# Kernel optimization log

Hardware: AMD Instinct MI355X
Metric: run time of the kernel (lower is better)

Reference implementation:

```python
import jax, jax.numpy as jnp
import numpy as np

N = 20000      # nodes
E = 320000     # edges (avg degree 16)
HID = 128      # hidden_channel
OUT = 128      # output_channel
SEQ = 8


def setup_inputs() -> dict:
    key = jax.random.key(0)
    ks = jax.random.split(key, 8)
    h = jax.random.normal(ks[0], (N, HID), jnp.float32)
    c = jax.random.normal(ks[1], (N, HID), jnp.float32)
    edge_index = jax.random.randint(ks[2], (2, E), 0, N, jnp.int64)
    edge_attr = jax.random.uniform(ks[3], (E,), jnp.float32)
    # GCNConv weights (PyG: x @ W then propagate), xavier-ish scale
    W_init = jax.random.normal(ks[4], (2 * HID, 2 * OUT), jnp.float32) * (2.0 / (2 * HID + 2 * OUT)) ** 0.5
    b_init = jnp.zeros((2 * OUT,), jnp.float32)
    W_cell = jax.random.normal(ks[5], (HID + OUT, 4 * OUT), jnp.float32) * (2.0 / (HID + OUT + 4 * OUT)) ** 0.5
    b_cell = jnp.zeros((4 * OUT,), jnp.float32)
    return {"h": h, "c": c, "edge_index": edge_index, "edge_attr": edge_attr,
            "W_init": W_init, "b_init": b_init, "W_cell": W_cell, "b_cell": b_cell,
            "seq_len": SEQ}


def _gcn(x, W, b, src, dst, ew, dinv):
    # PyG GCNConv with normalize=True, add_self_loops=True (self-loop weight 1.0)
    xw = x @ W                                   # [N, C_out]
    norm = dinv[src] * ew * dinv[dst]            # sym-normalized edge weights
    agg = jnp.zeros_like(xw).at[dst].add(xw[src] * norm[:, None])
    agg = agg + xw * (dinv * dinv)[:, None]      # self-loop term
    return agg + b


def reference(h, c, edge_index, edge_attr, W_init, b_init, W_cell, b_cell, seq_len):
    src, dst = edge_index[0], edge_index[1]
    n = h.shape[0]
    # degree with self-loops (weight 1.0), shared by both convs
    deg = jnp.zeros((n,), h.dtype).at[dst].add(edge_attr) + 1.0
    dinv = jax.lax.rsqrt(deg)

    # _init_states
    states = jax.nn.elu(_gcn(jnp.concatenate([h, c], axis=1), W_init, b_init, src, dst, edge_attr, dinv))
    h_t, c_t = states[:, :OUT], states[:, OUT:]

    def step(carry, _):
        h_cur, c_cur = carry
        # NOTE: original code feeds the initial h (not h_cur) as x each step
        combined = jnp.concatenate([h, h_cur], axis=1)
        cc = _gcn(combined, W_cell, b_cell, src, dst, edge_attr, dinv)
        cc_i, cc_f, cc_o, cc_g = jnp.split(cc, 4, axis=1)
        c_next = jax.nn.sigmoid(cc_f) * c_cur + jax.nn.sigmoid(cc_i) * jnp.tanh(cc_g)
        h_next = jax.nn.sigmoid(cc_o) * jnp.tanh(c_next)
        return (h_next, c_next), h_next

    (_, _), out = jax.lax.scan(step, (h_t, c_t), None, length=seq_len)
    return out  # [seq_len, N, OUT]
```

## Files before the change

kernel.cpp:

```cpp
#include <hip/hip_runtime.h>

#define N_NODES 20000
#define N_EDGES 320000
#define SEQ 8

typedef __attribute__((ext_vector_type(8))) short bf16x8;
typedef __attribute__((ext_vector_type(4))) float floatx4;
typedef const unsigned int __attribute__((address_space(1)))* gas_u32;
typedef unsigned int __attribute__((address_space(3)))* las_u32;

__device__ __forceinline__ unsigned short f2bf(float f) {
  unsigned int u = __builtin_bit_cast(unsigned int, f);
  return (unsigned short)((u + 0x7fffu + ((u >> 16) & 1u)) >> 16);
}
__device__ __forceinline__ float bflo(unsigned int u) {
  return __builtin_bit_cast(float, u << 16);
}
__device__ __forceinline__ float bfhi(unsigned int u) {
  return __builtin_bit_cast(float, u & 0xffff0000u);
}
__device__ __forceinline__ float sigf(float x) { return 1.f / (1.f + __expf(-x)); }

__device__ __forceinline__ void gl_lds16(const void* g, void* l) {
  auto gp = (gas_u32)g;
  auto lp = (las_u32)(unsigned int)(unsigned long long)l;
  __builtin_amdgcn_global_load_lds(gp, lp, 16, 0, 0);
}


__global__ void k_prologue(const float* __restrict__ Wi,
                           const float* __restrict__ Wc,
                           const float* __restrict__ bc,
                           unsigned short* __restrict__ WiT,
                           unsigned short* __restrict__ W1T,
                           unsigned short* __restrict__ W2T,
                           float* __restrict__ bcp,
                           float* __restrict__ deg, int* __restrict__ counts) {
  int idx = blockIdx.x * 256 + threadIdx.x;
  if (idx < N_NODES) { deg[idx] = 1.0f; counts[idx] = 0; }
  if (idx < 65536) {
    int n = idx >> 8, k = idx & 255;
    WiT[n * 256 + k] = f2bf(Wi[k * 256 + n]);
  }
  if (idx < 512) bcp[idx] = bc[((idx & 3) << 7) | (idx >> 2)];
  int n2 = idx >> 8, k2 = idx & 255;
  if (k2 < 128) {
    int orig = ((n2 & 3) << 7) | (n2 >> 2);
    W1T[n2 * 128 + k2] = f2bf(Wc[k2 * 512 + orig]);
    W2T[n2 * 128 + k2] = f2bf(Wc[(k2 + 128) * 512 + orig]);
  }
}

__global__ void k_deg(const int* __restrict__ ei, const float* __restrict__ ea,
                      float* __restrict__ deg, int* __restrict__ counts) {
  int e = blockIdx.x * 256 + threadIdx.x;
  if (e >= N_EDGES) return;
  int d = ei[N_EDGES + e];
  atomicAdd(&deg[d], ea[e]);
  atomicAdd(&counts[d], 1);
}

__global__ __launch_bounds__(1024) void k_scan(
    const int* __restrict__ counts, const float* __restrict__ deg,
    float* __restrict__ dinv, int* __restrict__ row_ptr,
    int* __restrict__ cursor) {
  __shared__ int sm[1024];
  int t = threadIdx.x;
  int base = t * 20;
  int local[20];
  int s = 0;
#pragma unroll
  for (int i = 0; i < 20; ++i) {
    int g = base + i;
    int v = (g < N_NODES) ? counts[g] : 0;
    local[i] = v;
    s += v;
  }
  sm[t] = s;
  __syncthreads();
  for (int o = 1; o < 1024; o <<= 1) {
    int add = (t >= o) ? sm[t - o] : 0;
    __syncthreads();
    sm[t] += add;
    __syncthreads();
  }
  int run = sm[t] - s;
#pragma unroll
  for (int i = 0; i < 20; ++i) {
    int g = base + i;
    if (g < N_NODES) {
      row_ptr[g] = run;
      cursor[g] = run;
      dinv[g] = rsqrtf(deg[g]);
    }
    run += local[i];
  }
  if (t == 0) row_ptr[N_NODES] = N_EDGES;
}

__global__ void k_fill(const int* __restrict__ ei, const float* __restrict__ ea,
                       const float* __restrict__ dinv, int* __restrict__ cursor,
                       int* __restrict__ csr_src, float* __restrict__ csr_w) {
  int e = blockIdx.x * 256 + threadIdx.x;
  if (e >= N_EDGES) return;
  int s = ei[e], d = ei[N_EDGES + e];
  int k = atomicAdd(&cursor[d], 1);
  csr_src[k] = s;
  csr_w[k] = dinv[s] * ea[e] * dinv[d];
}


__global__ __launch_bounds__(256) void k_agg_init(
    const float* __restrict__ h, const float* __restrict__ c,
    unsigned int* __restrict__ AhAc_u, const float* __restrict__ dinv,
    const int* __restrict__ row_ptr, const int* __restrict__ csr_src,
    const float* __restrict__ csr_w) {
  int wid = (blockIdx.x * 256 + threadIdx.x) >> 6;
  int lane = threadIdx.x & 63;
  if (wid >= N_NODES) return;
  float di = dinv[wid], dd = di * di;
  const float4* xb = (lane < 32) ? (const float4*)h : (const float4*)c;
  int lcol = lane & 31;
  float4 a = xb[(size_t)wid * 32 + lcol];
  float s0 = a.x * dd, s1 = a.y * dd, s2 = a.z * dd, s3 = a.w * dd;
  int e0 = row_ptr[wid], end = row_ptr[wid + 1];
  for (int base = e0; base < end; base += 64) {
    int n = end - base;
    if (n > 64) n = 64;
    int sl = 0;
    float wl = 0.f;
    if (base + lane < end) {
      sl = csr_src[base + lane];
      wl = csr_w[base + lane];
    }
    int j = 0;
    for (; j + 4 <= n; j += 4) {
      int sa = __shfl(sl, j), sb = __shfl(sl, j + 1);
      int sc = __shfl(sl, j + 2), sd = __shfl(sl, j + 3);
      float wa = __shfl(wl, j), wb = __shfl(wl, j + 1);
      float wc = __shfl(wl, j + 2), wd = __shfl(wl, j + 3);
      float4 va = xb[(size_t)sa * 32 + lcol];
      float4 vb = xb[(size_t)sb * 32 + lcol];
      float4 vc = xb[(size_t)sc * 32 + lcol];
      float4 vd = xb[(size_t)sd * 32 + lcol];
      s0 += va.x * wa; s1 += va.y * wa; s2 += va.z * wa; s3 += va.w * wa;
      s0 += vb.x * wb; s1 += vb.y * wb; s2 += vb.z * wb; s3 += vb.w * wb;
      s0 += vc.x * wc; s1 += vc.y * wc; s2 += vc.z * wc; s3 += vc.w * wc;
      s0 += vd.x * wd; s1 += vd.y * wd; s2 += vd.z * wd; s3 += vd.w * wd;
    }
    for (; j < n; ++j) {
      int sa = __shfl(sl, j);
      float wa = __shfl(wl, j);
      float4 va = xb[(size_t)sa * 32 + lcol];
      s0 += va.x * wa; s1 += va.y * wa; s2 += va.z * wa; s3 += va.w * wa;
    }
  }
  uint2 o;
  o.x = (unsigned int)f2bf(s0) | ((unsigned int)f2bf(s1) << 16);
  o.y = (unsigned int)f2bf(s2) | ((unsigned int)f2bf(s3) << 16);
  ((uint2*)AhAc_u)[(size_t)wid * 64 + lane] = o;
}

__global__ __launch_bounds__(256) void k_agg_step(
    const unsigned int* __restrict__ hbf_u, unsigned int* __restrict__ Aht_u,
    const float* __restrict__ dinv, const int* __restrict__ row_ptr,
    const int* __restrict__ csr_src, const float* __restrict__ csr_w) {
  int wid = (blockIdx.x * 256 + threadIdx.x) >> 6;
  int lane = threadIdx.x & 63;
  if (wid >= N_NODES) return;
  float di = dinv[wid], dd = di * di;
  unsigned int a = hbf_u[(size_t)wid * 64 + lane];
  float s0 = bflo(a) * dd, s1 = bfhi(a) * dd;
  int e0 = row_ptr[wid], end = row_ptr[wid + 1];
  for (int base = e0; base < end; base += 64) {
    int n = end - base;
    if (n > 64) n = 64;
    int sl = 0;
    float wl = 0.f;
    if (base + lane < end) {
      sl = csr_src[base + lane];
      wl = csr_w[base + lane];
    }
    int j = 0;
    for (; j + 4 <= n; j += 4) {
      int sa = __shfl(sl, j), sb = __shfl(sl, j + 1);
      int sc = __shfl(sl, j + 2), sd = __shfl(sl, j + 3);
      float wa = __shfl(wl, j), wb = __shfl(wl, j + 1);
      float wc = __shfl(wl, j + 2), wd = __shfl(wl, j + 3);
      unsigned int va = hbf_u[(size_t)sa * 64 + lane];
      unsigned int vb = hbf_u[(size_t)sb * 64 + lane];
      unsigned int vc = hbf_u[(size_t)sc * 64 + lane];
      unsigned int vd = hbf_u[(size_t)sd * 64 + lane];
      s0 += bflo(va) * wa; s1 += bfhi(va) * wa;
      s0 += bflo(vb) * wb; s1 += bfhi(vb) * wb;
      s0 += bflo(vc) * wc; s1 += bfhi(vc) * wc;
      s0 += bflo(vd) * wd; s1 += bfhi(vd) * wd;
    }
    for (; j < n; ++j) {
      int sa = __shfl(sl, j);
      float wa = __shfl(wl, j);
      unsigned int va = hbf_u[(size_t)sa * 64 + lane];
      s0 += bflo(va) * wa; s1 += bfhi(va) * wa;
    }
  }
  Aht_u[(size_t)wid * 64 + lane] =
      (unsigned int)f2bf(s0) | ((unsigned int)f2bf(s1) << 16);
}

template <int EPI, int KK, int LDA>
__global__ __launch_bounds__(256) void k_gemm(
    const unsigned short* __restrict__ A, const unsigned short* __restrict__ BT,
    const float* __restrict__ bias, const float* __restrict__ Kbuf,
    float* __restrict__ c_cur, unsigned short* __restrict__ hbf,
    float* __restrict__ out0) {
  __shared__ __align__(16) union {
    struct { unsigned short a[128 * 64]; unsigned short b[128 * 64]; } ab;
    float ep[64 * 132];
  } sm;
  const int M = N_NODES;
  int tid = threadIdx.x;
  int bm0 = blockIdx.x * 128, bn0 = blockIdx.y * 128;
  int wave = tid >> 6, lane = tid & 63;
  int wrow = (wave >> 1) * 64, wcol = (wave & 1) * 64;
  int lr = lane & 15, lq = lane >> 4;
  int key = lr & 7;

  int lr8 = lane >> 3, cq = lane & 7;
  int gq8 = (cq ^ lr8) * 8;

  floatx4 acc[4][4];
#pragma unroll
  for (int i = 0; i < 4; i++)
#pragma unroll
    for (int j = 0; j < 4; j++) acc[i][j] = (floatx4){0.f, 0.f, 0.f, 0.f};

  for (int k0 = 0; k0 < KK; k0 += 64) {
    __syncthreads();
#pragma unroll
    for (int p = 0; p < 4; ++p) {
      int row = p * 32 + wave * 8;
      int ra = bm0 + row + lr8;
      if (ra > M - 1) ra = M - 1;
      gl_lds16(A + (size_t)ra * LDA + k0 + gq8, sm.ab.a + row * 64);
      gl_lds16(BT + (size_t)(bn0 + row + lr8) * KK + k0 + gq8,
               sm.ab.b + row * 64);
    }
    __syncthreads();
#pragma unroll
    for (int ks = 0; ks < 2; ++ks) {
      int q = ks * 4 + lq;
      int slot = (q ^ key) << 3;
      bf16x8 af[4], bfr[4];
#pragma unroll
      for (int mi = 0; mi < 4; mi++)
        af[mi] = *(const bf16x8*)(sm.ab.a + (wrow + mi * 16 + lr) * 64 + slot);
#pragma unroll
      for (int ni = 0; ni < 4; ni++)
        bfr[ni] = *(const bf16x8*)(sm.ab.b + (wcol + ni * 16 + lr) * 64 + slot);
#pragma unroll
      for (int mi = 0; mi < 4; mi++)
#pragma unroll
        for (int ni = 0; ni < 4; ni++)
          acc[mi][ni] = __builtin_amdgcn_mfma_f32_16x16x32_bf16(
              af[mi], bfr[ni], acc[mi][ni], 0, 0, 0);
    }
  }
  __syncthreads();

  if (EPI == 0) {
#pragma unroll
    for (int mi = 0; mi < 4; mi++) {
#pragma unroll
      for (int r = 0; r < 4; r++) {
        int grow = bm0 + wrow + mi * 16 + lq * 4 + r;
        if (grow >= M) continue;
#pragma unroll
        for (int ni = 0; ni < 4; ni++) {
          int gcol = bn0 + wcol + ni * 16 + lr;
          float v = acc[mi][ni][r] + bias[gcol];
          v = (v > 0.f) ? v : expm1f(v);
          if (gcol < 128) hbf[(size_t)grow * 128 + gcol] = f2bf(v);
          else c_cur[(size_t)grow * 128 + gcol - 128] = v;
        }
      }
    }
  } else if (EPI == 1) {
#pragma unroll
    for (int mi = 0; mi < 4; mi++) {
#pragma unroll
      for (int r = 0; r < 4; r++) {
        int grow = bm0 + wrow + mi * 16 + lq * 4 + r;
        if (grow >= M) continue;
#pragma unroll
        for (int ni = 0; ni < 4; ni++) {
          int gcol = bn0 + wcol + ni * 16 + lr;
          out0[(size_t)grow * 512 + gcol] = acc[mi][ni][r] + bias[gcol];
        }
      }
    }
  } else {
#pragma unroll
    for (int hch = 0; hch < 2; ++hch) {
      if ((wrow >> 6) == hch) {
#pragma unroll
        for (int mi = 0; mi < 4; mi++)
#pragma unroll
          for (int r = 0; r < 4; r++) {
            int row_l = mi * 16 + lq * 4 + r;
#pragma unroll
            for (int ni = 0; ni < 4; ni++)
              sm.ep[row_l * 132 + wcol + ni * 16 + lr] = acc[mi][ni][r];
          }
      }
      __syncthreads();
#pragma unroll
      for (int it = 0; it < 8; ++it) {
        int p = tid + it * 256;
        int row_l = p >> 5, j = p & 31;
        int grow = bm0 + hch * 64 + row_l;
        if (grow < M) {
          int jg = (bn0 >> 2) + j;
          const float* eb = sm.ep + row_l * 132 + 4 * j;
          float4 kb = *(const float4*)&Kbuf[(size_t)grow * 512 + bn0 + 4 * j];
          float gi = eb[0] + kb.x;
          float gf = eb[1] + kb.y;
          float go = eb[2] + kb.z;
          float gg = eb[3] + kb.w;
          size_t o = (size_t)grow * 128 + jg;
          float cp = c_cur[o];
          float cn = sigf(gf) * cp + sigf(gi) * tanhf(gg);
          float hn = sigf(go) * tanhf(cn);
          c_cur[o] = cn;
          hbf[o] = f2bf(hn);
          out0[o] = hn;
        }
      }
      __syncthreads();
    }
  }
}

extern "C" void kernel_launch(void* const* d_in, const int* in_sizes, int n_in,
                              void* d_out, int out_size, void* d_ws, size_t ws_size,
                              hipStream_t stream) {
  const float* h  = (const float*)d_in[0];
  const float* c  = (const float*)d_in[1];
  const int*   ei = (const int*)d_in[2];
  const float* ea = (const float*)d_in[3];
  const float* Wi = (const float*)d_in[4];
  const float* bi = (const float*)d_in[5];
  const float* Wc = (const float*)d_in[6];
  const float* bc = (const float*)d_in[7];
  float* out = (float*)d_out;

  char* w = (char*)d_ws;
  size_t off = 0;
  auto alloc = [&](size_t bytes) {
    void* p = w + off;
    off += (bytes + 511) & ~(size_t)511;
    return p;
  };
  float* deg           = (float*)alloc(N_NODES * 4);
  float* dinv          = (float*)alloc(N_NODES * 4);
  int* counts          = (int*)alloc(N_NODES * 4);
  int* cursor          = (int*)alloc(N_NODES * 4);
  int* row_ptr         = (int*)alloc((N_NODES + 1) * 4);
  int* csr_src         = (int*)alloc(N_EDGES * 4);
  float* csr_w         = (float*)alloc(N_EDGES * 4);
  unsigned short* WiT  = (unsigned short*)alloc(256 * 256 * 2);
  unsigned short* W1T  = (unsigned short*)alloc(512 * 128 * 2);
  unsigned short* W2T  = (unsigned short*)alloc(512 * 128 * 2);
  float* bcp           = (float*)alloc(512 * 4);
  unsigned short* AhAc = (unsigned short*)alloc((size_t)N_NODES * 256 * 2);
  unsigned short* Aht  = (unsigned short*)alloc((size_t)N_NODES * 128 * 2);
  unsigned short* hbf  = (unsigned short*)alloc((size_t)N_NODES * 128 * 2);
  float* c_cur         = (float*)alloc((size_t)N_NODES * 128 * 4);
  float* Kbuf          = (float*)alloc((size_t)N_NODES * 512 * 4);

  const int NB_E = (N_EDGES + 255) / 256;
  const int NB_AGG = N_NODES * 64 / 256;
  const int MB = (N_NODES + 127) / 128;

  k_prologue<<<512, 256, 0, stream>>>(Wi, Wc, bc, WiT, W1T, W2T, bcp, deg,
                                      counts);
  k_deg<<<NB_E, 256, 0, stream>>>(ei, ea, deg, counts);
  k_scan<<<1, 1024, 0, stream>>>(counts, deg, dinv, row_ptr, cursor);
  k_fill<<<NB_E, 256, 0, stream>>>(ei, ea, dinv, cursor, csr_src, csr_w);

  k_agg_init<<<NB_AGG, 256, 0, stream>>>(h, c, (unsigned int*)AhAc, dinv,
                                         row_ptr, csr_src, csr_w);
  k_gemm<0, 256, 256><<<dim3(MB, 2), 256, 0, stream>>>(
      AhAc, WiT, bi, nullptr, c_cur, hbf, nullptr);
  k_gemm<1, 128, 256><<<dim3(MB, 4), 256, 0, stream>>>(
      AhAc, W1T, bcp, nullptr, nullptr, nullptr, Kbuf);

  for (int t = 0; t < SEQ; ++t) {
    k_agg_step<<<NB_AGG, 256, 0, stream>>>((unsigned int*)hbf,
                                           (unsigned int*)Aht, dinv, row_ptr,
                                           csr_src, csr_w);
    k_gemm<2, 128, 128><<<dim3(MB, 4), 256, 0, stream>>>(
        Aht, W2T, nullptr, Kbuf, c_cur, hbf, out + (size_t)t * N_NODES * 128);
  }
}
```

Measured before the change: 539.1 us.

## Pack CSR src/weight pairs, use scalar edge loads, stage GEMM K in 128 chunks

Interleaves each edge's source index and normalized weight into a single int2 array. The aggregation kernels now read edges with wave-uniform loads and readfirstlane, replacing per-lane loads followed by shuffles. The GEMM now loads two 64-wide K slices into LDS per barrier pair, which halves the number of syncthreads at the cost of doubling LDS for A/B tiles. That extra LDS may reduce occupancy.

```diff
diff --git a/kernel.cpp b/kernel.cpp
--- a/kernel.cpp
+++ b/kernel.cpp
@@ -100,61 +100,53 @@
 
 __global__ void k_fill(const int* __restrict__ ei, const float* __restrict__ ea,
                        const float* __restrict__ dinv, int* __restrict__ cursor,
-                       int* __restrict__ csr_src, float* __restrict__ csr_w) {
+                       int2* __restrict__ csr) {
   int e = blockIdx.x * 256 + threadIdx.x;
   if (e >= N_EDGES) return;
   int s = ei[e], d = ei[N_EDGES + e];
   int k = atomicAdd(&cursor[d], 1);
-  csr_src[k] = s;
-  csr_w[k] = dinv[s] * ea[e] * dinv[d];
+  int2 p;
+  p.x = s;
+  p.y = __builtin_bit_cast(int, dinv[s] * ea[e] * dinv[d]);
+  csr[k] = p;
 }
 
 
 __global__ __launch_bounds__(256) void k_agg_init(
     const float* __restrict__ h, const float* __restrict__ c,
     unsigned int* __restrict__ AhAc_u, const float* __restrict__ dinv,
-    const int* __restrict__ row_ptr, const int* __restrict__ csr_src,
-    const float* __restrict__ csr_w) {
-  int wid = (blockIdx.x * 256 + threadIdx.x) >> 6;
+    const int* __restrict__ row_ptr, const int2* __restrict__ csr) {
   int lane = threadIdx.x & 63;
+  int wid =
+      __builtin_amdgcn_readfirstlane((blockIdx.x * 256 + threadIdx.x) >> 6);
   if (wid >= N_NODES) return;
   float di = dinv[wid], dd = di * di;
   const float4* xb = (lane < 32) ? (const float4*)h : (const float4*)c;
   int lcol = lane & 31;
   float4 a = xb[(size_t)wid * 32 + lcol];
   float s0 = a.x * dd, s1 = a.y * dd, s2 = a.z * dd, s3 = a.w * dd;
-  int e0 = row_ptr[wid], end = row_ptr[wid + 1];
-  for (int base = e0; base < end; base += 64) {
-    int n = end - base;
-    if (n > 64) n = 64;
-    int sl = 0;
-    float wl = 0.f;
-    if (base + lane < end) {
-      sl = csr_src[base + lane];
-      wl = csr_w[base + lane];
-    }
-    int j = 0;
-    for (; j + 4 <= n; j += 4) {
-      int sa = __shfl(sl, j), sb = __shfl(sl, j + 1);
-      int sc = __shfl(sl, j + 2), sd = __shfl(sl, j + 3);
-      float wa = __shfl(wl, j), wb = __shfl(wl, j + 1);
-      float wc = __shfl(wl, j + 2), wd = __shfl(wl, j + 3);
-      float4 va = xb[(size_t)sa * 32 + lcol];
-      float4 vb = xb[(size_t)sb * 32 + lcol];
-      float4 vc = xb[(size_t)sc * 32 + lcol];
-      float4 vd = xb[(size_t)sd * 32 + lcol];
-      s0 += va.x * wa; s1 += va.y * wa; s2 += va.z * wa; s3 += va.w * wa;
-      s0 += vb.x * wb; s1 += vb.y * wb; s2 += vb.z * wb; s3 += vb.w * wb;
-      s0 += vc.x * wc; s1 += vc.y * wc; s2 += vc.z * wc; s3 += vc.w * wc;
-      s0 += vd.x * wd; s1 += vd.y * wd; s2 += vd.z * wd; s3 += vd.w * wd;
-    }
-    for (; j < n; ++j) {
-      int sa = __shfl(sl, j);
-      float wa = __shfl(wl, j);
-      float4 va = xb[(size_t)sa * 32 + lcol];
-      s0 += va.x * wa; s1 += va.y * wa; s2 += va.z * wa; s3 += va.w * wa;
-    }
-  }
+  int e0 = __builtin_amdgcn_readfirstlane(row_ptr[wid]);
+  int end = __builtin_amdgcn_readfirstlane(row_ptr[wid + 1]);
+
+#define EDGE_I(P)                                                        \
+  {                                                                      \
+    int sidx = __builtin_amdgcn_readfirstlane((P).x);                    \
+    float wv = __builtin_bit_cast(                                       \
+        float, __builtin_amdgcn_readfirstlane((P).y));                   \
+    float4 v = xb[(size_t)sidx * 32 + lcol];                             \
+    s0 += v.x * wv; s1 += v.y * wv; s2 += v.z * wv; s3 += v.w * wv;      \
+  }
+
+  int j = e0;
+  for (; j + 4 <= end; j += 4) {
+    int2 p0 = csr[j], p1 = csr[j + 1], p2 = csr[j + 2], p3 = csr[j + 3];
+    EDGE_I(p0) EDGE_I(p1) EDGE_I(p2) EDGE_I(p3)
+  }
+  for (; j < end; ++j) {
+    int2 p = csr[j];
+    EDGE_I(p)
+  }
+#undef EDGE_I
   uint2 o;
   o.x = (unsigned int)f2bf(s0) | ((unsigned int)f2bf(s1) << 16);
   o.y = (unsigned int)f2bf(s2) | ((unsigned int)f2bf(s3) << 16);
@@ -164,45 +156,36 @@
 __global__ __launch_bounds__(256) void k_agg_step(
     const unsigned int* __restrict__ hbf_u, unsigned int* __restrict__ Aht_u,
     const float* __restrict__ dinv, const int* __restrict__ row_ptr,
-    const int* __restrict__ csr_src, const float* __restrict__ csr_w) {
-  int wid = (blockIdx.x * 256 + threadIdx.x) >> 6;
+    const int2* __restrict__ csr) {
   int lane = threadIdx.x & 63;
+  int wid =
+      __builtin_amdgcn_readfirstlane((blockIdx.x * 256 + threadIdx.x) >> 6);
   if (wid >= N_NODES) return;
   float di = dinv[wid], dd = di * di;
   unsigned int a = hbf_u[(size_t)wid * 64 + lane];
   float s0 = bflo(a) * dd, s1 = bfhi(a) * dd;
-  int e0 = row_ptr[wid], end = row_ptr[wid + 1];
-  for (int base = e0; base < end; base += 64) {
-    int n = end - base;
-    if (n > 64) n = 64;
-    int sl = 0;
-    float wl = 0.f;
-    if (base + lane < end) {
-      sl = csr_src[base + lane];
-      wl = csr_w[base + lane];
-    }
-    int j = 0;
-    for (; j + 4 <= n; j += 4) {
-      int sa = __shfl(sl, j), sb = __shfl(sl, j + 1);
-      int sc = __shfl(sl, j + 2), sd = __shfl(sl, j + 3);
-      float wa = __shfl(wl, j), wb = __shfl(wl, j + 1);
-      float wc = __shfl(wl, j + 2), wd = __shfl(wl, j + 3);
-      unsigned int va = hbf_u[(size_t)sa * 64 + lane];
-      unsigned int vb = hbf_u[(size_t)sb * 64 + lane];
-      unsigned int vc = hbf_u[(size_t)sc * 64 + lane];
-      unsigned int vd = hbf_u[(size_t)sd * 64 + lane];
-      s0 += bflo(va) * wa; s1 += bfhi(va) * wa;
-      s0 += bflo(vb) * wb; s1 += bfhi(vb) * wb;
-      s0 += bflo(vc) * wc; s1 += bfhi(vc) * wc;
-      s0 += bflo(vd) * wd; s1 += bfhi(vd) * wd;
-    }
-    for (; j < n; ++j) {
-      int sa = __shfl(sl, j);
-      float wa = __shfl(wl, j);
-      unsigned int va = hbf_u[(size_t)sa * 64 + lane];
-      s0 += bflo(va) * wa; s1 += bfhi(va) * wa;
-    }
-  }
+  int e0 = __builtin_amdgcn_readfirstlane(row_ptr[wid]);
+  int end = __builtin_amdgcn_readfirstlane(row_ptr[wid + 1]);
+
+#define EDGE_S(P)                                                        \
+  {                                                                      \
+    int sidx = __builtin_amdgcn_readfirstlane((P).x);                    \
+    float wv = __builtin_bit_cast(                                       \
+        float, __builtin_amdgcn_readfirstlane((P).y));                   \
+    unsigned int v = hbf_u[(size_t)sidx * 64 + lane];                    \
+    s0 += bflo(v) * wv; s1 += bfhi(v) * wv;                              \
+  }
+
+  int j = e0;
+  for (; j + 4 <= end; j += 4) {
+    int2 p0 = csr[j], p1 = csr[j + 1], p2 = csr[j + 2], p3 = csr[j + 3];
+    EDGE_S(p0) EDGE_S(p1) EDGE_S(p2) EDGE_S(p3)
+  }
+  for (; j < end; ++j) {
+    int2 p = csr[j];
+    EDGE_S(p)
+  }
+#undef EDGE_S
   Aht_u[(size_t)wid * 64 + lane] =
       (unsigned int)f2bf(s0) | ((unsigned int)f2bf(s1) << 16);
 }
@@ -214,7 +197,10 @@
     float* __restrict__ c_cur, unsigned short* __restrict__ hbf,
     float* __restrict__ out0) {
   __shared__ __align__(16) union {
-    struct { unsigned short a[128 * 64]; unsigned short b[128 * 64]; } ab;
+    struct {
+      unsigned short a[2][128 * 64];
+      unsigned short b[2][128 * 64];
+    } ab;
     float ep[64 * 132];
   } sm;
   const int M = N_NODES;
@@ -234,35 +220,44 @@
 #pragma unroll
     for (int j = 0; j < 4; j++) acc[i][j] = (floatx4){0.f, 0.f, 0.f, 0.f};
 
-  for (int k0 = 0; k0 < KK; k0 += 64) {
+  for (int k0 = 0; k0 < KK; k0 += 128) {
+    if (k0) __syncthreads();
+#pragma unroll
+    for (int half = 0; half < 2; ++half) {
+      int kk = k0 + half * 64;
+#pragma unroll
+      for (int p = 0; p < 4; ++p) {
+        int row = p * 32 + wave * 8;
+        int ra = bm0 + row + lr8;
+        if (ra > M - 1) ra = M - 1;
+        gl_lds16(A + (size_t)ra * LDA + kk + gq8, sm.ab.a[half] + row * 64);
+        gl_lds16(BT + (size_t)(bn0 + row + lr8) * KK + kk + gq8,
+                 sm.ab.b[half] + row * 64);
+      }
+    }
     __syncthreads();
 #pragma unroll
-    for (int p = 0; p < 4; ++p) {
-      int row = p * 32 + wave * 8;
-      int ra = bm0 + row + lr8;
-      if (ra > M - 1) ra = M - 1;
-      gl_lds16(A + (size_t)ra * LDA + k0 + gq8, sm.ab.a + row * 64);
-      gl_lds16(BT + (size_t)(bn0 + row + lr8) * KK + k0 + gq8,
-               sm.ab.b + row * 64);
-    }
-    __syncthreads();
-#pragma unroll
-    for (int ks = 0; ks < 2; ++ks) {
-      int q = ks * 4 + lq;
-      int slot = (q ^ key) << 3;
-      bf16x8 af[4], bfr[4];
-#pragma unroll
-      for (int mi = 0; mi < 4; mi++)
-        af[mi] = *(const bf16x8*)(sm.ab.a + (wrow + mi * 16 + lr) * 64 + slot);
-#pragma unroll
-      for (int ni = 0; ni < 4; ni++)
-        bfr[ni] = *(const bf16x8*)(sm.ab.b + (wcol + ni * 16 + lr) * 64 + slot);
-#pragma unroll
-      for (int mi = 0; mi < 4; mi++)
+    for (int half = 0; half < 2; ++half) {
+#pragma unroll
+      for (int ks = 0; ks < 2; ++ks) {
+        int q = ks * 4 + lq;
+        int slot = (q ^ key) << 3;
+        bf16x8 af[4], bfr[4];
+#pragma unroll
+        for (int mi = 0; mi < 4; mi++)
+          af[mi] =
+              *(const bf16x8*)(sm.ab.a[half] + (wrow + mi * 16 + lr) * 64 + slot);
 #pragma unroll
         for (int ni = 0; ni < 4; ni++)
-          acc[mi][ni] = __builtin_amdgcn_mfma_f32_16x16x32_bf16(
-              af[mi], bfr[ni], acc[mi][ni], 0, 0, 0);
+          bfr[ni] =
+              *(const bf16x8*)(sm.ab.b[half] + (wcol + ni * 16 + lr) * 64 + slot);
+#pragma unroll
+        for (int mi = 0; mi < 4; mi++)
+#pragma unroll
+          for (int ni = 0; ni < 4; ni++)
+            acc[mi][ni] = __builtin_amdgcn_mfma_f32_16x16x32_bf16(
+                af[mi], bfr[ni], acc[mi][ni], 0, 0, 0);
+      }
     }
   }
   __syncthreads();
@@ -365,8 +360,7 @@
   int* counts          = (int*)alloc(N_NODES * 4);
   int* cursor          = (int*)alloc(N_NODES * 4);
   int* row_ptr         = (int*)alloc((N_NODES + 1) * 4);
-  int* csr_src         = (int*)alloc(N_EDGES * 4);
-  float* csr_w         = (float*)alloc(N_EDGES * 4);
+  int2* csr            = (int2*)alloc((size_t)N_EDGES * 8);
   unsigned short* WiT  = (unsigned short*)alloc(256 * 256 * 2);
   unsigned short* W1T  = (unsigned short*)alloc(512 * 128 * 2);
   unsigned short* W2T  = (unsigned short*)alloc(512 * 128 * 2);
@@ -385,10 +379,10 @@
                                       counts);
   k_deg<<<NB_E, 256, 0, stream>>>(ei, ea, deg, counts);
   k_scan<<<1, 1024, 0, stream>>>(counts, deg, dinv, row_ptr, cursor);
-  k_fill<<<NB_E, 256, 0, stream>>>(ei, ea, dinv, cursor, csr_src, csr_w);
+  k_fill<<<NB_E, 256, 0, stream>>>(ei, ea, dinv, cursor, csr);
 
   k_agg_init<<<NB_AGG, 256, 0, stream>>>(h, c, (unsigned int*)AhAc, dinv,
-                                         row_ptr, csr_src, csr_w);
+                                         row_ptr, csr);
   k_gemm<0, 256, 256><<<dim3(MB, 2), 256, 0, stream>>>(
       AhAc, WiT, bi, nullptr, c_cur, hbf, nullptr);
   k_gemm<1, 128, 256><<<dim3(MB, 4), 256, 0, stream>>>(
@@ -397,7 +391,7 @@
   for (int t = 0; t < SEQ; ++t) {
     k_agg_step<<<NB_AGG, 256, 0, stream>>>((unsigned int*)hbf,
                                            (unsigned int*)Aht, dinv, row_ptr,
-                                           csr_src, csr_w);
+                                           csr);
     k_gemm<2, 128, 128><<<dim3(MB, 4), 256, 0, stream>>>(
         Aht, W2T, nullptr, Kbuf, c_cur, hbf, out + (size_t)t * N_NODES * 128);
   }
```

Measured after the change: 605.2 us. 1.12x slower.

## Fold constant-input GEMM into per-step K=256 GEMM, pack CSR, warp-scan

Applied to the files above, without the earlier changes.

The per-step gate GEMM now runs with K=256 over [A·h, A·h_t], with the cell bias applied in the epilogue. Previously, the part that depends on the initial h was precomputed once into a large fp32 Kbuf and read back every step. The aggregation step writes A·h_t into the second half of the AhAc buffer, so the Kbuf allocation and its per-step traffic go away, at the cost of doubling MFMA work per step. CSR source indices and weights are packed into one int2 array, so each edge needs one load instead of two. The single-block scan uses wave shuffles and vectorized loads and stores in place of a barrier-heavy LDS scan.

```diff
diff --git a/kernel.cpp b/kernel.cpp
--- a/kernel.cpp
+++ b/kernel.cpp
@@ -32,8 +32,7 @@
                            const float* __restrict__ Wc,
                            const float* __restrict__ bc,
                            unsigned short* __restrict__ WiT,
-                           unsigned short* __restrict__ W1T,
-                           unsigned short* __restrict__ W2T,
+                           unsigned short* __restrict__ WcT,
                            float* __restrict__ bcp,
                            float* __restrict__ deg, int* __restrict__ counts) {
   int idx = blockIdx.x * 256 + threadIdx.x;
@@ -44,11 +43,8 @@
   }
   if (idx < 512) bcp[idx] = bc[((idx & 3) << 7) | (idx >> 2)];
   int n2 = idx >> 8, k2 = idx & 255;
-  if (k2 < 128) {
-    int orig = ((n2 & 3) << 7) | (n2 >> 2);
-    W1T[n2 * 128 + k2] = f2bf(Wc[k2 * 512 + orig]);
-    W2T[n2 * 128 + k2] = f2bf(Wc[(k2 + 128) * 512 + orig]);
-  }
+  int orig = ((n2 & 3) << 7) | (n2 >> 2);
+  WcT[n2 * 256 + k2] = f2bf(Wc[k2 * 512 + orig]);
 }
 
 __global__ void k_deg(const int* __restrict__ ei, const float* __restrict__ ea,
@@ -64,57 +60,87 @@
     const int* __restrict__ counts, const float* __restrict__ deg,
     float* __restrict__ dinv, int* __restrict__ row_ptr,
     int* __restrict__ cursor) {
-  __shared__ int sm[1024];
+  __shared__ int smw[16];
   int t = threadIdx.x;
+  int lane = t & 63, wv = t >> 6;
   int base = t * 20;
-  int local[20];
+  int v[20];
+  float dv[20];
+  bool live = (t < 1000);
+  if (live) {
+    const int4* pc = (const int4*)(counts + base);
+    const float4* pd = (const float4*)(deg + base);
+#pragma unroll
+    for (int i = 0; i < 5; ++i) {
+      int4 q = pc[i];
+      float4 f = pd[i];
+      v[4 * i] = q.x; v[4 * i + 1] = q.y; v[4 * i + 2] = q.z; v[4 * i + 3] = q.w;
+      dv[4 * i] = f.x; dv[4 * i + 1] = f.y; dv[4 * i + 2] = f.z; dv[4 * i + 3] = f.w;
+    }
+  } else {
+#pragma unroll
+    for (int i = 0; i < 20; ++i) { v[i] = 0; dv[i] = 1.f; }
+  }
   int s = 0;
 #pragma unroll
-  for (int i = 0; i < 20; ++i) {
-    int g = base + i;
-    int v = (g < N_NODES) ? counts[g] : 0;
-    local[i] = v;
-    s += v;
-  }
-  sm[t] = s;
+  for (int i = 0; i < 20; ++i) s += v[i];
+  int inc = s;
+#pragma unroll
+  for (int o = 1; o < 64; o <<= 1) {
+    int u = __shfl_up(inc, o);
+    if (lane >= o) inc += u;
+  }
+  if (lane == 63) smw[wv] = inc;
   __syncthreads();
-  for (int o = 1; o < 1024; o <<= 1) {
-    int add = (t >= o) ? sm[t - o] : 0;
-    __syncthreads();
-    sm[t] += add;
-    __syncthreads();
-  }
-  int run = sm[t] - s;
-#pragma unroll
-  for (int i = 0; i < 20; ++i) {
-    int g = base + i;
-    if (g < N_NODES) {
-      row_ptr[g] = run;
-      cursor[g] = run;
-      dinv[g] = rsqrtf(deg[g]);
-    }
-    run += local[i];
+  if (t == 0) {
+    int r = 0;
+#pragma unroll
+    for (int i = 0; i < 16; ++i) { int x = smw[i]; smw[i] = r; r += x; }
+  }
+  __syncthreads();
+  int run = smw[wv] + inc - s;
+  if (live) {
+    int rp[20];
+    float iv[20];
+#pragma unroll
+    for (int i = 0; i < 20; ++i) {
+      rp[i] = run;
+      run += v[i];
+      iv[i] = rsqrtf(dv[i]);
+    }
+    int4* prp = (int4*)(row_ptr + base);
+    int4* pcu = (int4*)(cursor + base);
+    float4* pdv = (float4*)(dinv + base);
+#pragma unroll
+    for (int i = 0; i < 5; ++i) {
+      int4 q; q.x = rp[4 * i]; q.y = rp[4 * i + 1]; q.z = rp[4 * i + 2]; q.w = rp[4 * i + 3];
+      prp[i] = q;
+      pcu[i] = q;
+      float4 f; f.x = iv[4 * i]; f.y = iv[4 * i + 1]; f.z = iv[4 * i + 2]; f.w = iv[4 * i + 3];
+      pdv[i] = f;
+    }
   }
   if (t == 0) row_ptr[N_NODES] = N_EDGES;
 }
 
 __global__ void k_fill(const int* __restrict__ ei, const float* __restrict__ ea,
                        const float* __restrict__ dinv, int* __restrict__ cursor,
-                       int* __restrict__ csr_src, float* __restrict__ csr_w) {
+                       int2* __restrict__ csr) {
   int e = blockIdx.x * 256 + threadIdx.x;
   if (e >= N_EDGES) return;
   int s = ei[e], d = ei[N_EDGES + e];
   int k = atomicAdd(&cursor[d], 1);
-  csr_src[k] = s;
-  csr_w[k] = dinv[s] * ea[e] * dinv[d];
+  int2 p;
+  p.x = s;
+  p.y = __builtin_bit_cast(int, dinv[s] * ea[e] * dinv[d]);
+  csr[k] = p;
 }
 
 
 __global__ __launch_bounds__(256) void k_agg_init(
     const float* __restrict__ h, const float* __restrict__ c,
     unsigned int* __restrict__ AhAc_u, const float* __restrict__ dinv,
-    const int* __restrict__ row_ptr, const int* __restrict__ csr_src,
-    const float* __restrict__ csr_w) {
+    const int* __restrict__ row_ptr, const int2* __restrict__ csr) {
   int wid = (blockIdx.x * 256 + threadIdx.x) >> 6;
   int lane = threadIdx.x & 63;
   if (wid >= N_NODES) return;
@@ -130,8 +156,9 @@
     int sl = 0;
     float wl = 0.f;
     if (base + lane < end) {
-      sl = csr_src[base + lane];
-      wl = csr_w[base + lane];
+      int2 p = csr[base + lane];
+      sl = p.x;
+      wl = __builtin_bit_cast(float, p.y);
     }
     int j = 0;
     for (; j + 4 <= n; j += 4) {
@@ -162,9 +189,9 @@
 }
 
 __global__ __launch_bounds__(256) void k_agg_step(
-    const unsigned int* __restrict__ hbf_u, unsigned int* __restrict__ Aht_u,
+    const unsigned int* __restrict__ hbf_u, unsigned int* __restrict__ AhAc_u,
     const float* __restrict__ dinv, const int* __restrict__ row_ptr,
-    const int* __restrict__ csr_src, const float* __restrict__ csr_w) {
+    const int2* __restrict__ csr) {
   int wid = (blockIdx.x * 256 + threadIdx.x) >> 6;
   int lane = threadIdx.x & 63;
   if (wid >= N_NODES) return;
@@ -178,8 +205,9 @@
     int sl = 0;
     float wl = 0.f;
     if (base + lane < end) {
-      sl = csr_src[base + lane];
-      wl = csr_w[base + lane];
+      int2 p = csr[base + lane];
+      sl = p.x;
+      wl = __builtin_bit_cast(float, p.y);
     }
     int j = 0;
     for (; j + 4 <= n; j += 4) {
@@ -203,14 +231,14 @@
       s0 += bflo(va) * wa; s1 += bfhi(va) * wa;
     }
   }
-  Aht_u[(size_t)wid * 64 + lane] =
+  AhAc_u[(size_t)wid * 128 + 64 + lane] =
       (unsigned int)f2bf(s0) | ((unsigned int)f2bf(s1) << 16);
 }
 
 template <int EPI, int KK, int LDA>
 __global__ __launch_bounds__(256) void k_gemm(
     const unsigned short* __restrict__ A, const unsigned short* __restrict__ BT,
-    const float* __restrict__ bias, const float* __restrict__ Kbuf,
+    const float* __restrict__ bias,
     float* __restrict__ c_cur, unsigned short* __restrict__ hbf,
     float* __restrict__ out0) {
   __shared__ __align__(16) union {
@@ -284,20 +312,6 @@
         }
       }
     }
-  } else if (EPI == 1) {
-#pragma unroll
-    for (int mi = 0; mi < 4; mi++) {
-#pragma unroll
-      for (int r = 0; r < 4; r++) {
-        int grow = bm0 + wrow + mi * 16 + lq * 4 + r;
-        if (grow >= M) continue;
-#pragma unroll
-        for (int ni = 0; ni < 4; ni++) {
-          int gcol = bn0 + wcol + ni * 16 + lr;
-          out0[(size_t)grow * 512 + gcol] = acc[mi][ni][r] + bias[gcol];
-        }
-      }
-    }
   } else {
 #pragma unroll
     for (int hch = 0; hch < 2; ++hch) {
@@ -321,7 +335,7 @@
         if (grow < M) {
           int jg = (bn0 >> 2) + j;
           const float* eb = sm.ep + row_l * 132 + 4 * j;
-          float4 kb = *(const float4*)&Kbuf[(size_t)grow * 512 + bn0 + 4 * j];
+          float4 kb = *(const float4*)&bias[bn0 + 4 * j];
           float gi = eb[0] + kb.x;
           float gf = eb[1] + kb.y;
           float go = eb[2] + kb.z;
@@ -365,40 +379,33 @@
   int* counts          = (int*)alloc(N_NODES * 4);
   int* cursor          = (int*)alloc(N_NODES * 4);
   int* row_ptr         = (int*)alloc((N_NODES + 1) * 4);
-  int* csr_src         = (int*)alloc(N_EDGES * 4);
-  float* csr_w         = (float*)alloc(N_EDGES * 4);
+  int2* csr            = (int2*)alloc((size_t)N_EDGES * 8);
   unsigned short* WiT  = (unsigned short*)alloc(256 * 256 * 2);
-  unsigned short* W1T  = (unsigned short*)alloc(512 * 128 * 2);
-  unsigned short* W2T  = (unsigned short*)alloc(512 * 128 * 2);
+  unsigned short* WcT  = (unsigned short*)alloc(512 * 256 * 2);
   float* bcp           = (float*)alloc(512 * 4);
   unsigned short* AhAc = (unsigned short*)alloc((size_t)N_NODES * 256 * 2);
-  unsigned short* Aht  = (unsigned short*)alloc((size_t)N_NODES * 128 * 2);
   unsigned short* hbf  = (unsigned short*)alloc((size_t)N_NODES * 128 * 2);
   float* c_cur         = (float*)alloc((size_t)N_NODES * 128 * 4);
-  float* Kbuf          = (float*)alloc((size_t)N_NODES * 512 * 4);
 
   const int NB_E = (N_EDGES + 255) / 256;
   const int NB_AGG = N_NODES * 64 / 256;
   const int MB = (N_NODES + 127) / 128;
 
-  k_prologue<<<512, 256, 0, stream>>>(Wi, Wc, bc, WiT, W1T, W2T, bcp, deg,
-                                      counts);
+  k_prologue<<<512, 256, 0, stream>>>(Wi, Wc, bc, WiT, WcT, bcp, deg, counts);
   k_deg<<<NB_E, 256, 0, stream>>>(ei, ea, deg, counts);
   k_scan<<<1, 1024, 0, stream>>>(counts, deg, dinv, row_ptr, cursor);
-  k_fill<<<NB_E, 256, 0, stream>>>(ei, ea, dinv, cursor, csr_src, csr_w);
+  k_fill<<<NB_E, 256, 0, stream>>>(ei, ea, dinv, cursor, csr);
 
   k_agg_init<<<NB_AGG, 256, 0, stream>>>(h, c, (unsigned int*)AhAc, dinv,
-                                         row_ptr, csr_src, csr_w);
+                                         row_ptr, csr);
   k_gemm<0, 256, 256><<<dim3(MB, 2), 256, 0, stream>>>(
-      AhAc, WiT, bi, nullptr, c_cur, hbf, nullptr);
-  k_gemm<1, 128, 256><<<dim3(MB, 4), 256, 0, stream>>>(
-      AhAc, W1T, bcp, nullptr, nullptr, nullptr, Kbuf);
+      AhAc, WiT, bi, c_cur, hbf, nullptr);
 
   for (int t = 0; t < SEQ; ++t) {
     k_agg_step<<<NB_AGG, 256, 0, stream>>>((unsigned int*)hbf,
-                                           (unsigned int*)Aht, dinv, row_ptr,
-                                           csr_src, csr_w);
-    k_gemm<2, 128, 128><<<dim3(MB, 4), 256, 0, stream>>>(
-        Aht, W2T, nullptr, Kbuf, c_cur, hbf, out + (size_t)t * N_NODES * 128);
-  }
-}
+                                           (unsigned int*)AhAc, dinv, row_ptr,
+                                           csr);
+    k_gemm<2, 256, 256><<<dim3(MB, 4), 256, 0, stream>>>(
+        AhAc, WcT, bcp, c_cur, hbf, out + (size_t)t * N_NODES * 128);
+  }
+}
```

Measured after the change: 508.9 us. 5.6% less time.
